# Kernel optimization log

Hardware: AMD Instinct MI355X
Metric: run time of the kernel (lower is better)

## Reference

```python
import jax, jax.numpy as jnp
import numpy as np

THRESH = 0.2  # contact probability threshold from _make_graph default


def setup_inputs() -> dict:
    key = jax.random.key(0)
    ks = jax.random.split(key, 10)
    L, D, K, M = 1024, 640, 32, 64
    S = jax.random.normal(ks[0], (L, D), jnp.float32)
    P = jax.random.uniform(ks[1], (L, L), jnp.float32)
    P = 0.5 * (P + P.T)  # symmetric base-pair probability matrix
    xyz = jax.random.normal(ks[2], (L, 3), jnp.float32) * 10.0  # Angstrom-scale C1' coords
    rbf_mu = jnp.linspace(0.0, 30.0, K).astype(jnp.float32)     # RBF centers over 0-30 A
    rbf_sigma = jax.random.uniform(ks[3], (K,), jnp.float32, 0.5, 2.0)
    W_edge = jax.random.normal(ks[4], (K + 2, M), jnp.float32) * 0.05
    b_edge = jnp.zeros((M,), jnp.float32)
    W_node = jax.random.normal(ks[5], (D, M), jnp.float32) * 0.05
    w_out = jax.random.normal(ks[6], (M,), jnp.float32) * 0.1
    return {"S": S, "P": P, "xyz": xyz, "rbf_mu": rbf_mu, "rbf_sigma": rbf_sigma,
            "W_edge": W_edge, "b_edge": b_edge, "W_node": W_node, "w_out": w_out}


def reference(S, P, xyz, rbf_mu, rbf_sigma, W_edge, b_edge, W_node, w_out):
    """Graph construction (_make_graph) + one SE3-style gated coordinate update.

    Edges: backbone (j == i+1, etype=0, pij=1) and high-prob contacts
    (P[i,j] > THRESH, j > i+2, etype=1, pij=P[i,j]). Edge scalars are
    [etype, pij, rbf(d)] exactly as in _make_graph; edge vectors are
    xyz[j]-xyz[i]. Computed in dense masked form for jit-compatibility.
    """
    L = xyz.shape[0]
    rel = xyz[None, :, :] - xyz[:, None, :]                      # (L,L,3) xyz[j]-xyz[i]
    # safe norm: eps avoids nan grad on zero diagonal (diagonal is masked out anyway)
    d = jnp.sqrt(jnp.sum(rel * rel, axis=-1, keepdims=True) + 1e-12)  # (L,L,1)
    rbf_feat = jnp.exp(-(d - rbf_mu) ** 2 / (2.0 * rbf_sigma ** 2))   # (L,L,K)

    idx = jnp.arange(L)
    backbone = idx[None, :] == idx[:, None] + 1                  # j == i+1
    contact = (P > THRESH) & (idx[None, :] > idx[:, None] + 2)   # skip j <= i+2
    mask = backbone | contact                                    # (L,L)

    etype = contact.astype(S.dtype)                              # 0 backbone, 1 contact
    pij = jnp.where(backbone, jnp.asarray(1.0, S.dtype), P)
    e_scalar = jnp.concatenate([etype[..., None], pij[..., None], rbf_feat], axis=-1)  # (L,L,K+2)

    # gather-compute: message from edge scalars + destination-node scalars
    node_proj = S @ W_node                                       # (L,M)
    msg = jax.nn.relu(jnp.einsum('ijk,km->ijm', e_scalar, W_edge) + b_edge
                      + node_proj[None, :, :])                   # (L,L,M)
    gate = jax.nn.sigmoid(msg @ w_out) * mask.astype(S.dtype)    # (L,L)

    # scatter: equivariant coordinate update, sum of gated edge vectors per node
    xyz_out = xyz + jnp.einsum('ij,ijc->ic', gate, rel)          # (L,3)
    return xyz_out
```

## Files before the change

### kernel.cpp

```cpp
#include <hip/hip_runtime.h>
#include <math.h>

#define LL 1024
#define DD 640
#define KK 32
#define MM 64
#define THRESH 0.2f
#define LOG2E 1.4426950408889634f

#define NPROJ_OFF  0
#define NPROJC_OFF (NPROJ_OFF + LL * MM)
#define WRT_OFF    (NPROJC_OFF + LL * MM)
#define W1_OFF     (WRT_OFF + 1024)
#define EA_OFF     (W1_OFF + MM)
#define EB_OFF     (EA_OFF + KK)
#define EC_OFF     (EB_OFF + KK)
#define XYZ4_OFF   (EC_OFF + KK)

typedef float f32x4_t __attribute__((ext_vector_type(4)));
typedef short bf16x8_t __attribute__((ext_vector_type(8)));

union FragU { unsigned int u[4]; bf16x8_t v; };

#if __has_builtin(__builtin_amdgcn_sqrtf)
#define FSQRT __builtin_amdgcn_sqrtf
#else
#define FSQRT sqrtf
#endif

#if __has_builtin(__builtin_amdgcn_exp2f)
#define EXP2F __builtin_amdgcn_exp2f
#else
#define EXP2F(x) __expf((x) * 0.6931471805599453f)
#endif

__device__ __forceinline__ unsigned int pack_bf(float hi, float lo) {
    return __builtin_amdgcn_perm(__float_as_uint(hi), __float_as_uint(lo), 0x07060302u);
}

__global__ __launch_bounds__(256) void prep_sk(
    const float* __restrict__ S, const float* __restrict__ xyz,
    const float* __restrict__ rbf_mu, const float* __restrict__ rbf_sigma,
    const float* __restrict__ W_edge, const float* __restrict__ b_edge,
    const float* __restrict__ W_node, float* __restrict__ ws,
    float* __restrict__ out)
{
    const int b = blockIdx.x;
    const int t = threadIdx.x;
    if (b < 256) {
        __shared__ float red[4][64][4];
        const int lane = t & 63;
        const int wave = t >> 6;
        const int r0   = (b >> 2) * 16;
        const int n0   = (b & 3) * 16;
        const int col  = lane & 15;
        const int quad = lane >> 4;

        f32x4_t acc = {0.f, 0.f, 0.f, 0.f};
        const float* arow = S + (size_t)(r0 + col) * DD + wave * 160 + quad * 8;
        const float* bcol = W_node + (size_t)(wave * 160 + quad * 8) * MM + n0 + col;

        #pragma unroll
        for (int ks = 0; ks < 5; ++ks) {
            const float4 a0 = *(const float4*)(arow + ks * 32);
            const float4 a1 = *(const float4*)(arow + ks * 32 + 4);
            FragU A;
            A.u[0] = pack_bf(a0.y, a0.x); A.u[1] = pack_bf(a0.w, a0.z);
            A.u[2] = pack_bf(a1.y, a1.x); A.u[3] = pack_bf(a1.w, a1.z);
            const float* bk = bcol + (size_t)ks * 32 * MM;
            const float b0 = bk[0 * MM], b1 = bk[1 * MM], b2 = bk[2 * MM], b3 = bk[3 * MM];
            const float b4 = bk[4 * MM], b5 = bk[5 * MM], b6 = bk[6 * MM], b7 = bk[7 * MM];
            FragU B;
            B.u[0] = pack_bf(b1, b0); B.u[1] = pack_bf(b3, b2);
            B.u[2] = pack_bf(b5, b4); B.u[3] = pack_bf(b7, b6);
            acc = __builtin_amdgcn_mfma_f32_16x16x32_bf16(A.v, B.v, acc, 0, 0, 0);
        }
        red[wave][lane][0] = acc[0];
        red[wave][lane][1] = acc[1];
        red[wave][lane][2] = acc[2];
        red[wave][lane][3] = acc[3];
        __syncthreads();
        const int lr  = t & 63;
        const int reg = t >> 6;
        const float v = (red[0][lr][reg] + red[1][lr][reg])
                      + (red[2][lr][reg] + red[3][lr][reg]);
        const int row = r0 + (lr >> 4) * 4 + reg;
        const int cc  = n0 + (lr & 15);
        const float vb = v + b_edge[cc];
        ws[NPROJ_OFF  + (size_t)row * MM + cc] = vb;
        ws[NPROJC_OFF + (size_t)row * MM + cc] = vb + W_edge[cc];
    } else {
        unsigned short* wrt = (unsigned short*)(ws + WRT_OFF);
        if (t < MM) ws[W1_OFF + t] = W_edge[MM + t];
        if (t < KK) {
            const float s  = rbf_sigma[t];
            const float m_ = rbf_mu[t];
            const float inv = 1.0f / (2.0f * s * s);
            ws[EA_OFF + t] = -LOG2E * inv;
            ws[EB_OFF + t] =  2.0f * LOG2E * inv * m_;
            ws[EC_OFF + t] = -LOG2E * inv * m_ * m_;
        }
        for (int idx = t; idx < KK * MM; idx += 256) {
            const int m = idx >> 5, k = idx & 31;
            unsigned int u = __float_as_uint(W_edge[(2 + k) * MM + m]);
            u = (u + 0x7fffu + ((u >> 16) & 1u)) >> 16;
            wrt[idx] = (unsigned short)u;
        }
        for (int n = t; n < LL; n += 256) {
            float4 v;
            v.x = xyz[3 * n + 0]; v.y = xyz[3 * n + 1];
            v.z = xyz[3 * n + 2]; v.w = 0.0f;
            *(float4*)(ws + XYZ4_OFF + 4 * n) = v;
        }
        for (int idx = t; idx < 3 * LL; idx += 256) out[idx] = xyz[idx];
    }
}

__global__ __launch_bounds__(256, 4) void edge_kernel5(
    const float* __restrict__ P, const float* __restrict__ w_out,
    const float* __restrict__ ws, float* __restrict__ out)
{
    const int tid  = threadIdx.x;
    const int lane = tid & 63;
    const int wave = tid >> 6;
    const int quad = lane >> 4;
    const int col  = lane & 15;
    __shared__ float sred[4][3];

    const float* __restrict__ nproj  = ws + NPROJ_OFF;
    const float* __restrict__ nprojc = ws + NPROJC_OFF;
    const float4* __restrict__ xyz4  = (const float4*)(ws + XYZ4_OFF);
    const unsigned short* __restrict__ wrt = (const unsigned short*)(ws + WRT_OFF);

    FragU ar[4];
    float w1r[16], wvr[16];
    float aj[8], bj[8], cj[8];
    #pragma unroll
    for (int mt = 0; mt < 4; ++mt) {
        const uint4 w = *(const uint4*)(wrt + (mt * 16 + col) * KK + quad * 8);
        ar[mt].u[0] = w.x; ar[mt].u[1] = w.y; ar[mt].u[2] = w.z; ar[mt].u[3] = w.w;
        const f32x4_t w1 = *(const f32x4_t*)(ws + W1_OFF + mt * 16 + quad * 4);
        const f32x4_t wo = *(const f32x4_t*)(w_out + mt * 16 + quad * 4);
        #pragma unroll
        for (int r = 0; r < 4; ++r) { w1r[mt * 4 + r] = w1[r]; wvr[mt * 4 + r] = wo[r]; }
    }
    #pragma unroll
    for (int j = 0; j < 8; ++j) {
        aj[j] = ws[EA_OFF + quad * 8 + j];
        bj[j] = ws[EB_OFF + quad * 8 + j];
        cj[j] = ws[EC_OFF + quad * 8 + j];
    }

    const int b = (int)blockIdx.x;

    #pragma unroll 1
    for (int ss = 0; ss < 2; ++ss) {
        int i, s0, s1;
        if (ss == 0) {
            i = b;
            const int len = (LL - 1) - b;
            s0 = 0; s1 = (len + 1) >> 1;
        } else {
            i = (LL - 1) - b;
            const int len = b;
            s0 = (len + 1) >> 1; s1 = len;
        }
        const float4 xo = xyz4[i];
        const float xi0 = xo.x, xi1 = xo.y, xi2 = xo.z;
        float ax = 0.f, ay = 0.f, az = 0.f;
        const float* __restrict__ prow = P + (size_t)i * LL;

        for (int base = s0 + wave * 64; base < s1; base += 256) {
            const int jo = base + lane;
            const bool valid = jo < s1;
            const int jc_o = valid ? (i + 1 + jo) : (LL - 1);
            const float p_own = prow[jc_o];
            const float4 xj = xyz4[jc_o];
            const float rx = xj.x - xi0, ry = xj.y - xi1, rz = xj.z - xi2;
            const bool msk = valid && ((jo == 0) || ((jo >= 2) && (p_own > THRESH)));

            float res[4];
            #pragma unroll
            for (int ct = 0; ct < 4; ++ct) {
                const int jo_n = base + ct * 16 + col;
                int jc = i + 1 + jo_n;
                jc = (jc < LL) ? jc : (LL - 1);
                const float p_n = prow[jc];
                const float4 xn = xyz4[jc];
                const float dx = xn.x - xi0, dy = xn.y - xi1, dz = xn.z - xi2;
                const float q2 = fmaf(dx, dx, fmaf(dy, dy, fmaf(dz, dz, 1e-12f)));
                const float d_n = FSQRT(q2);
                const bool bb = (jo_n == 0);
                const float peff = bb ? 1.0f : p_n;
                const float* npr = (bb ? nproj : nprojc) + (size_t)jc * MM;

                float e[8];
                #pragma unroll
                for (int j = 0; j < 8; ++j)
                    e[j] = EXP2F(fmaf(aj[j], q2, fmaf(bj[j], d_n, cj[j])));
                FragU bf;
                bf.u[0] = pack_bf(e[1], e[0]); bf.u[1] = pack_bf(e[3], e[2]);
                bf.u[2] = pack_bf(e[5], e[4]); bf.u[3] = pack_bf(e[7], e[6]);

                float g = 0.0f;
                #pragma unroll
                for (int mt = 0; mt < 4; ++mt) {
                    f32x4_t c0 = *(const f32x4_t*)(npr + mt * 16 + quad * 4);
                    c0[0] = fmaf(peff, w1r[mt*4+0], c0[0]);
                    c0[1] = fmaf(peff, w1r[mt*4+1], c0[1]);
                    c0[2] = fmaf(peff, w1r[mt*4+2], c0[2]);
                    c0[3] = fmaf(peff, w1r[mt*4+3], c0[3]);
                    c0 = __builtin_amdgcn_mfma_f32_16x16x32_bf16(ar[mt].v, bf.v, c0, 0, 0, 0);
                    g = fmaf(fmaxf(c0[0], 0.f), wvr[mt*4+0], g);
                    g = fmaf(fmaxf(c0[1], 0.f), wvr[mt*4+1], g);
                    g = fmaf(fmaxf(c0[2], 0.f), wvr[mt*4+2], g);
                    g = fmaf(fmaxf(c0[3], 0.f), wvr[mt*4+3], g);
                }
                g += __shfl_xor(g, 16, 64);
                g += __shfl_xor(g, 32, 64);
                res[ct] = g;
            }
            float gd = res[0];
            gd = (quad == 1) ? res[1] : gd;
            gd = (quad == 2) ? res[2] : gd;
            gd = (quad == 3) ? res[3] : gd;
            const float gate = msk ? (1.0f / (1.0f + __expf(-gd))) : 0.0f;
            ax = fmaf(gate, rx, ax);
            ay = fmaf(gate, ry, ay);
            az = fmaf(gate, rz, az);
        }

        #pragma unroll
        for (int off = 32; off > 0; off >>= 1) {
            ax += __shfl_down(ax, off, 64);
            ay += __shfl_down(ay, off, 64);
            az += __shfl_down(az, off, 64);
        }
        if (lane == 0) { sred[wave][0] = ax; sred[wave][1] = ay; sred[wave][2] = az; }
        __syncthreads();
        if (tid == 0) {
            const float tx = (sred[0][0] + sred[1][0]) + (sred[2][0] + sred[3][0]);
            const float ty = (sred[0][1] + sred[1][1]) + (sred[2][1] + sred[3][1]);
            const float tz = (sred[0][2] + sred[1][2]) + (sred[2][2] + sred[3][2]);
            atomicAdd(out + i * 3 + 0, tx);
            atomicAdd(out + i * 3 + 1, ty);
            atomicAdd(out + i * 3 + 2, tz);
        }
        __syncthreads();
    }
}

extern "C" void kernel_launch(void* const* d_in, const int* in_sizes, int n_in,
                              void* d_out, int out_size, void* d_ws, size_t ws_size,
                              hipStream_t stream) {
    const float* S         = (const float*)d_in[0];
    const float* P         = (const float*)d_in[1];
    const float* xyz       = (const float*)d_in[2];
    const float* rbf_mu    = (const float*)d_in[3];
    const float* rbf_sigma = (const float*)d_in[4];
    const float* W_edge    = (const float*)d_in[5];
    const float* b_edge    = (const float*)d_in[6];
    const float* W_node    = (const float*)d_in[7];
    const float* w_out     = (const float*)d_in[8];
    float* out = (float*)d_out;
    float* ws  = (float*)d_ws;

    prep_sk<<<257, 256, 0, stream>>>(S, xyz, rbf_mu, rbf_sigma,
                                     W_edge, b_edge, W_node, ws, out);
    edge_kernel5<<<LL, 256, 0, stream>>>(P, w_out, ws, out);
}
```

Measured before the change: 101.1 us.

## Assign one row per block, stage xyz in LDS, drop atomics

Replaces the paired-row load-balanced scheme with one block per row i, so each block owns its full output and writes xyz+sum directly instead of using atomicAdd. The copy of xyz into out is removed from the prep kernel, and coordinates are staged into shared memory per block. Launch bounds no longer request 4 blocks per CU. Work per block now varies linearly with the row index, which risks load imbalance and a longer tail.

```diff
diff --git a/kernel.cpp b/kernel.cpp
--- a/kernel.cpp
+++ b/kernel.cpp
@@ -42,8 +42,7 @@
     const float* __restrict__ S, const float* __restrict__ xyz,
     const float* __restrict__ rbf_mu, const float* __restrict__ rbf_sigma,
     const float* __restrict__ W_edge, const float* __restrict__ b_edge,
-    const float* __restrict__ W_node, float* __restrict__ ws,
-    float* __restrict__ out)
+    const float* __restrict__ W_node, float* __restrict__ ws)
 {
     const int b = blockIdx.x;
     const int t = threadIdx.x;
@@ -112,11 +111,10 @@
             v.z = xyz[3 * n + 2]; v.w = 0.0f;
             *(float4*)(ws + XYZ4_OFF + 4 * n) = v;
         }
-        for (int idx = t; idx < 3 * LL; idx += 256) out[idx] = xyz[idx];
-    }
-}
-
-__global__ __launch_bounds__(256, 4) void edge_kernel5(
+    }
+}
+
+__global__ __launch_bounds__(256) void edge_kernel6(
     const float* __restrict__ P, const float* __restrict__ w_out,
     const float* __restrict__ ws, float* __restrict__ out)
 {
@@ -125,12 +123,16 @@
     const int wave = tid >> 6;
     const int quad = lane >> 4;
     const int col  = lane & 15;
+    __shared__ float4 lxyz[LL];
     __shared__ float sred[4][3];
 
     const float* __restrict__ nproj  = ws + NPROJ_OFF;
     const float* __restrict__ nprojc = ws + NPROJC_OFF;
     const float4* __restrict__ xyz4  = (const float4*)(ws + XYZ4_OFF);
     const unsigned short* __restrict__ wrt = (const unsigned short*)(ws + WRT_OFF);
+
+    #pragma unroll
+    for (int n = tid; n < LL; n += 256) lxyz[n] = xyz4[n];
 
     FragU ar[4];
     float w1r[16], wvr[16];
@@ -150,103 +152,90 @@
         bj[j] = ws[EB_OFF + quad * 8 + j];
         cj[j] = ws[EC_OFF + quad * 8 + j];
     }
-
-    const int b = (int)blockIdx.x;
-
-    #pragma unroll 1
-    for (int ss = 0; ss < 2; ++ss) {
-        int i, s0, s1;
-        if (ss == 0) {
-            i = b;
-            const int len = (LL - 1) - b;
-            s0 = 0; s1 = (len + 1) >> 1;
-        } else {
-            i = (LL - 1) - b;
-            const int len = b;
-            s0 = (len + 1) >> 1; s1 = len;
-        }
-        const float4 xo = xyz4[i];
-        const float xi0 = xo.x, xi1 = xo.y, xi2 = xo.z;
-        float ax = 0.f, ay = 0.f, az = 0.f;
-        const float* __restrict__ prow = P + (size_t)i * LL;
-
-        for (int base = s0 + wave * 64; base < s1; base += 256) {
-            const int jo = base + lane;
-            const bool valid = jo < s1;
-            const int jc_o = valid ? (i + 1 + jo) : (LL - 1);
-            const float p_own = prow[jc_o];
-            const float4 xj = xyz4[jc_o];
-            const float rx = xj.x - xi0, ry = xj.y - xi1, rz = xj.z - xi2;
-            const bool msk = valid && ((jo == 0) || ((jo >= 2) && (p_own > THRESH)));
-
-            float res[4];
+    __syncthreads();
+
+    const int i = (int)blockIdx.x;
+    const float4 xo = lxyz[i];
+    const float xi0 = xo.x, xi1 = xo.y, xi2 = xo.z;
+    const int len = (LL - 1) - i;
+    float ax = 0.f, ay = 0.f, az = 0.f;
+    const float* __restrict__ prow = P + (size_t)i * LL;
+
+    for (int base = wave * 64; base < len; base += 256) {
+        const int jo = base + lane;
+        const bool valid = jo < len;
+        const int jc_o = valid ? (i + 1 + jo) : (LL - 1);
+        const float p_own = prow[jc_o];
+        const float4 xj = lxyz[jc_o];
+        const float rx = xj.x - xi0, ry = xj.y - xi1, rz = xj.z - xi2;
+        const bool msk = valid && ((jo == 0) || ((jo >= 2) && (p_own > THRESH)));
+
+        float res[4];
+        #pragma unroll
+        for (int ct = 0; ct < 4; ++ct) {
+            const int jo_n = base + ct * 16 + col;
+            int jc = i + 1 + jo_n;
+            jc = (jc < LL) ? jc : (LL - 1);
+            const float p_n = prow[jc];
+            const float4 xn = lxyz[jc];
+            const float dx = xn.x - xi0, dy = xn.y - xi1, dz = xn.z - xi2;
+            const float q2 = fmaf(dx, dx, fmaf(dy, dy, fmaf(dz, dz, 1e-12f)));
+            const float d_n = FSQRT(q2);
+            const bool bb = (jo_n == 0);
+            const float peff = bb ? 1.0f : p_n;
+            const float* npr = (bb ? nproj : nprojc) + (size_t)jc * MM;
+
+            float e[8];
             #pragma unroll
-            for (int ct = 0; ct < 4; ++ct) {
-                const int jo_n = base + ct * 16 + col;
-                int jc = i + 1 + jo_n;
-                jc = (jc < LL) ? jc : (LL - 1);
-                const float p_n = prow[jc];
-                const float4 xn = xyz4[jc];
-                const float dx = xn.x - xi0, dy = xn.y - xi1, dz = xn.z - xi2;
-                const float q2 = fmaf(dx, dx, fmaf(dy, dy, fmaf(dz, dz, 1e-12f)));
-                const float d_n = FSQRT(q2);
-                const bool bb = (jo_n == 0);
-                const float peff = bb ? 1.0f : p_n;
-                const float* npr = (bb ? nproj : nprojc) + (size_t)jc * MM;
-
-                float e[8];
-                #pragma unroll
-                for (int j = 0; j < 8; ++j)
-                    e[j] = EXP2F(fmaf(aj[j], q2, fmaf(bj[j], d_n, cj[j])));
-                FragU bf;
-                bf.u[0] = pack_bf(e[1], e[0]); bf.u[1] = pack_bf(e[3], e[2]);
-                bf.u[2] = pack_bf(e[5], e[4]); bf.u[3] = pack_bf(e[7], e[6]);
-
-                float g = 0.0f;
-                #pragma unroll
-                for (int mt = 0; mt < 4; ++mt) {
-                    f32x4_t c0 = *(const f32x4_t*)(npr + mt * 16 + quad * 4);
-                    c0[0] = fmaf(peff, w1r[mt*4+0], c0[0]);
-                    c0[1] = fmaf(peff, w1r[mt*4+1], c0[1]);
-                    c0[2] = fmaf(peff, w1r[mt*4+2], c0[2]);
-                    c0[3] = fmaf(peff, w1r[mt*4+3], c0[3]);
-                    c0 = __builtin_amdgcn_mfma_f32_16x16x32_bf16(ar[mt].v, bf.v, c0, 0, 0, 0);
-                    g = fmaf(fmaxf(c0[0], 0.f), wvr[mt*4+0], g);
-                    g = fmaf(fmaxf(c0[1], 0.f), wvr[mt*4+1], g);
-                    g = fmaf(fmaxf(c0[2], 0.f), wvr[mt*4+2], g);
-                    g = fmaf(fmaxf(c0[3], 0.f), wvr[mt*4+3], g);
-                }
-                g += __shfl_xor(g, 16, 64);
-                g += __shfl_xor(g, 32, 64);
-                res[ct] = g;
+            for (int j = 0; j < 8; ++j)
+                e[j] = EXP2F(fmaf(aj[j], q2, fmaf(bj[j], d_n, cj[j])));
+            FragU bf;
+            bf.u[0] = pack_bf(e[1], e[0]); bf.u[1] = pack_bf(e[3], e[2]);
+            bf.u[2] = pack_bf(e[5], e[4]); bf.u[3] = pack_bf(e[7], e[6]);
+
+            float g = 0.0f;
+            #pragma unroll
+            for (int mt = 0; mt < 4; ++mt) {
+                f32x4_t c0 = *(const f32x4_t*)(npr + mt * 16 + quad * 4);
+                c0[0] = fmaf(peff, w1r[mt*4+0], c0[0]);
+                c0[1] = fmaf(peff, w1r[mt*4+1], c0[1]);
+                c0[2] = fmaf(peff, w1r[mt*4+2], c0[2]);
+                c0[3] = fmaf(peff, w1r[mt*4+3], c0[3]);
+                c0 = __builtin_amdgcn_mfma_f32_16x16x32_bf16(ar[mt].v, bf.v, c0, 0, 0, 0);
+                g = fmaf(fmaxf(c0[0], 0.f), wvr[mt*4+0], g);
+                g = fmaf(fmaxf(c0[1], 0.f), wvr[mt*4+1], g);
+                g = fmaf(fmaxf(c0[2], 0.f), wvr[mt*4+2], g);
+                g = fmaf(fmaxf(c0[3], 0.f), wvr[mt*4+3], g);
             }
-            float gd = res[0];
-            gd = (quad == 1) ? res[1] : gd;
-            gd = (quad == 2) ? res[2] : gd;
-            gd = (quad == 3) ? res[3] : gd;
-            const float gate = msk ? (1.0f / (1.0f + __expf(-gd))) : 0.0f;
-            ax = fmaf(gate, rx, ax);
-            ay = fmaf(gate, ry, ay);
-            az = fmaf(gate, rz, az);
-        }
-
-        #pragma unroll
-        for (int off = 32; off > 0; off >>= 1) {
-            ax += __shfl_down(ax, off, 64);
-            ay += __shfl_down(ay, off, 64);
-            az += __shfl_down(az, off, 64);
-        }
-        if (lane == 0) { sred[wave][0] = ax; sred[wave][1] = ay; sred[wave][2] = az; }
-        __syncthreads();
-        if (tid == 0) {
-            const float tx = (sred[0][0] + sred[1][0]) + (sred[2][0] + sred[3][0]);
-            const float ty = (sred[0][1] + sred[1][1]) + (sred[2][1] + sred[3][1]);
-            const float tz = (sred[0][2] + sred[1][2]) + (sred[2][2] + sred[3][2]);
-            atomicAdd(out + i * 3 + 0, tx);
-            atomicAdd(out + i * 3 + 1, ty);
-            atomicAdd(out + i * 3 + 2, tz);
-        }
-        __syncthreads();
+            g += __shfl_xor(g, 16, 64);
+            g += __shfl_xor(g, 32, 64);
+            res[ct] = g;
+        }
+        float gd = res[0];
+        gd = (quad == 1) ? res[1] : gd;
+        gd = (quad == 2) ? res[2] : gd;
+        gd = (quad == 3) ? res[3] : gd;
+        const float gate = msk ? (1.0f / (1.0f + __expf(-gd))) : 0.0f;
+        ax = fmaf(gate, rx, ax);
+        ay = fmaf(gate, ry, ay);
+        az = fmaf(gate, rz, az);
+    }
+
+    #pragma unroll
+    for (int off = 32; off > 0; off >>= 1) {
+        ax += __shfl_down(ax, off, 64);
+        ay += __shfl_down(ay, off, 64);
+        az += __shfl_down(az, off, 64);
+    }
+    if (lane == 0) { sred[wave][0] = ax; sred[wave][1] = ay; sred[wave][2] = az; }
+    __syncthreads();
+    if (tid == 0) {
+        const float tx = (sred[0][0] + sred[1][0]) + (sred[2][0] + sred[3][0]);
+        const float ty = (sred[0][1] + sred[1][1]) + (sred[2][1] + sred[3][1]);
+        const float tz = (sred[0][2] + sred[1][2]) + (sred[2][2] + sred[3][2]);
+        out[i * 3 + 0] = xi0 + tx;
+        out[i * 3 + 1] = xi1 + ty;
+        out[i * 3 + 2] = xi2 + tz;
     }
 }
 
@@ -266,6 +255,6 @@
     float* ws  = (float*)d_ws;
 
     prep_sk<<<257, 256, 0, stream>>>(S, xyz, rbf_mu, rbf_sigma,
-                                     W_edge, b_edge, W_node, ws, out);
-    edge_kernel5<<<LL, 256, 0, stream>>>(P, w_out, ws, out);
-}
+                                     W_edge, b_edge, W_node, ws);
+    edge_kernel6<<<LL, 256, 0, stream>>>(P, w_out, ws, out);
+}
```

After: 100.8 us. Within noise of the previous version (-0.3%).
